# Performance work log

Hardware: AMD Instinct MI355X
Metric: run time of the kernel (lower is better)

The kernel has to match this reference:

```python
import jax, jax.numpy as jnp
import numpy as np

E = 128       # embed_dim
H = 128       # hidden_dim
NLABEL = 5
VOCAB = 50000
DEPTH = 18    # levels 0..17, complete binary tree
BRANCH = 2
N_NODES = 2 ** DEPTH - 1  # level-order layout: level l occupies [2^l-1, 2^(l+1)-1)


def setup_inputs() -> dict:
    key = jax.random.key(0)
    ks = jax.random.split(key, 24)

    def w(k, shape):
        return jax.random.normal(k, shape, dtype=jnp.float32) * 0.05

    inp = {
        "embeds": w(ks[0], (VOCAB, E)),
        "node_words": jax.random.randint(ks[1], (N_NODES,), 0, VOCAB),
        "node_labels": jax.random.randint(ks[2], (N_NODES,), 0, NLABEL),
        "depth": DEPTH,
        "branching": BRANCH,
    }
    # 8 gate linears: *x maps E->H, *h maps H->H (torch nn.Linear: y = x @ W.T + b)
    for j, nm in enumerate(["ix", "ih", "fx", "fh", "ox", "oh", "ux", "uh"]):
        in_dim = E if nm.endswith("x") else H
        inp["W" + nm] = w(ks[3 + 2 * j], (H, in_dim))
        inp["b" + nm] = w(ks[4 + 2 * j], (H,))
    inp["Wout"] = w(ks[20], (NLABEL, H))
    inp["bout"] = w(ks[21], (NLABEL,))
    return inp


def _lin(x, W, b):
    return x @ W.T + b


def _tree_lstm(embeds, node_words, node_labels, depth, branching,
               Wix, bix, Wih, bih, Wfx, bfx, Wfh, bfh,
               Wox, box, Woh, boh, Wux, bux, Wuh, buh, Wout, bout):
    b = branching
    hid = Wix.shape[0]
    loss = jnp.zeros((), dtype=embeds.dtype)
    child_c = child_h = None
    logp = None
    # bottom-up over levels (leaves first); level l has b^l nodes at offset (b^l-1)/(b-1)
    for l in range(depth - 1, -1, -1):
        n = b ** l
        off = (b ** l - 1) // (b - 1)
        x = embeds[node_words[off:off + n]]            # [n, E]
        if child_h is None:                            # leaves: zero child states
            h_sum = jnp.zeros((n, hid), dtype=embeds.dtype)
            c_agg = jnp.zeros((n, hid), dtype=embeds.dtype)
        else:
            ch = child_h.reshape(n, b, hid)            # children of each level-l node
            cc = child_c.reshape(n, b, hid)
            h_sum = ch.sum(axis=1)                     # child-sum
            f = jax.nn.sigmoid(_lin(x, Wfx, bfx)[:, None, :] + _lin(ch, Wfh, bfh))
            c_agg = (f * cc).sum(axis=1)               # sum_k f_k * c_k
        i = jax.nn.sigmoid(_lin(x, Wix, bix) + _lin(h_sum, Wih, bih))
        o = jax.nn.sigmoid(_lin(x, Wox, box) + _lin(h_sum, Woh, boh))
        u = jnp.tanh(_lin(x, Wux, bux) + _lin(h_sum, Wuh, buh))
        c = i * u + c_agg
        h = o * jnp.tanh(c)
        logp = jax.nn.log_softmax(_lin(h, Wout, bout), axis=-1)   # [n, NLABEL]
        lab = node_labels[off:off + n]
        loss = loss - logp[jnp.arange(n), lab].sum()              # NLL summed over nodes
        child_c, child_h = c, h
    return logp, loss  # logp from level 0 = root log-probs [1, NLABEL]


def reference(embeds, node_words, node_labels, depth, branching,
              Wix, bix, Wih, bih, Wfx, bfx, Wfh, bfh,
              Wox, box, Woh, boh, Wux, bux, Wuh, buh, Wout, bout):
    return _tree_lstm(embeds, node_words, node_labels, depth, branching,
                      Wix, bix, Wih, bih, Wfx, bfx, Wfh, bfh,
                      Wox, box, Woh, boh, Wux, bux, Wuh, buh, Wout, bout)
```

## Files before the change

### kernel.cpp

```cpp
#include <hip/hip_runtime.h>
#include <math.h>

#define DEPTH 18
#define NINT ((1 << (DEPTH - 1)) - 1)
#define LEAF_OFF ((1 << (DEPTH - 2)) - 1)
#define NVOCAB 50000
#define SAW 520
#define KTS 9

typedef unsigned short bf16raw;
typedef __bf16 bf16x8 __attribute__((ext_vector_type(8)));
typedef float f32x4 __attribute__((ext_vector_type(4)));
typedef short short8 __attribute__((ext_vector_type(8)));

__device__ __forceinline__ float sigm(float x) { return 1.0f / (1.0f + __expf(-x)); }
__device__ __forceinline__ float fast_tanh(float x) {
    float t = __expf(2.0f * x);
    return 1.0f - 2.0f / (t + 1.0f);
}

__device__ __forceinline__ float bf2f(bf16raw u) {
    union { unsigned int i; float f; } v;
    v.i = ((unsigned int)u) << 16;
    return v.f;
}
__device__ __forceinline__ bf16raw f2bf(float f) {
    union { float f; unsigned int i; } v;
    v.f = f;
    unsigned int r = v.i + 0x7FFFu + ((v.i >> 16) & 1u);
    return (bf16raw)(r >> 16);
}

#define SB() __builtin_amdgcn_sched_barrier(0)

__global__ __launch_bounds__(256) void k_prep_embeds(const float* __restrict__ src,
                                                     bf16raw* __restrict__ dst, int n4)
{
    int i = blockIdx.x * blockDim.x + threadIdx.x;
    if (i < n4) {
        float4 v = ((const float4*)src)[i];
        ushort4 o;
        o.x = f2bf(v.x); o.y = f2bf(v.y); o.z = f2bf(v.z); o.w = f2bf(v.w);
        ((ushort4*)dst)[i] = o;
    }
}

__global__ __launch_bounds__(128) void k_prep_bcat(
    const float* __restrict__ Wix, const float* __restrict__ bix,
    const float* __restrict__ Wih, const float* __restrict__ bih,
    const float* __restrict__ Wfx, const float* __restrict__ bfx,
    const float* __restrict__ Wfh, const float* __restrict__ bfh,
    const float* __restrict__ Wox, const float* __restrict__ box_,
    const float* __restrict__ Woh, const float* __restrict__ boh,
    const float* __restrict__ Wux, const float* __restrict__ bux,
    const float* __restrict__ Wuh, const float* __restrict__ buh,
    const float* __restrict__ Wout,
    bf16raw* __restrict__ Bfrag, bf16raw* __restrict__ WoutFrag,
    float* __restrict__ bias_cat)
{
    const int j = blockIdx.x;
    if (j >= 512) {
        const int col = j - 512;
        for (int k = threadIdx.x; k < 128; k += blockDim.x) {
            float v = (col < 5) ? Wout[col * 128 + k] : 0.f;
            WoutFrag[((k >> 5) * 64 + ((k >> 3) & 3) * 16 + col) * 8 + (k & 7)] = f2bf(v);
        }
        return;
    }
    const int gate = j >> 7, jj = j & 127;
    const float *Wx, *Wh, *bx, *bh;
    switch (gate) {
        case 0: Wx = Wix; Wh = Wih; bx = bix;  bh = bih; break;
        case 1: Wx = Wux; Wh = Wuh; bx = bux;  bh = buh; break;
        case 2: Wx = Wox; Wh = Woh; bx = box_; bh = boh; break;
        default: Wx = Wfx; Wh = Wfh; bx = bfx; bh = bfh; break;
    }
    const int coltile = (j >> 4) & 7, lr = j & 15;
    for (int k = threadIdx.x; k < 256; k += blockDim.x) {
        float v = (k < 128) ? Wx[jj * 128 + k] : Wh[jj * 128 + (k - 128)];
        const int idx = (((gate * 8 + coltile) * KTS + (k >> 5)) * 64
                         + ((k >> 3) & 3) * 16 + lr) * 8 + (k & 7);
        Bfrag[idx] = f2bf(v);
    }
    if (threadIdx.x == 0) bias_cat[j] = bx[jj] + bh[jj];
}

template<int CB>
__device__ __forceinline__ void lp_burst(const bf16raw* __restrict__ bfbase, int wcol,
                                         bf16x8 (&bb)[16])
{
#pragma unroll
    for (int kt = 0; kt < 4; ++kt)
#pragma unroll
        for (int j = 0; j < 4; ++j)
            bb[kt * 4 + j] = *(const bf16x8*)(bfbase +
                    (long)(((CB * 8 + (wcol >> 4) + j) * KTS + kt) * 512));
}

__device__ __forceinline__ void lp_mfma_all(const bf16raw* __restrict__ sA, int wrow,
                                            int lrow, int lquad,
                                            bf16x8 (&bb)[16], f32x4 (&acc)[2][4])
{
#pragma unroll
    for (int kt = 0; kt < 4; ++kt) {
        bf16x8 af[2];
#pragma unroll
        for (int i = 0; i < 2; ++i)
            af[i] = *(const bf16x8*)&sA[(wrow + i * 16 + lrow) * 136 + kt * 32 + lquad * 8];
#pragma unroll
        for (int i = 0; i < 2; ++i)
#pragma unroll
            for (int j = 0; j < 4; ++j)
                acc[i][j] = __builtin_amdgcn_mfma_f32_16x16x32_bf16(af[i], bb[kt * 4 + j], acc[i][j], 0, 0, 0);
    }
}

template<int CB>
__device__ __forceinline__ void lp_rungemm(const bf16raw* __restrict__ sA,
                                           const bf16raw* __restrict__ bfbase,
                                           int wrow, int wcol, int lrow, int lquad,
                                           f32x4 (&acc)[2][4])
{
#pragma unroll
    for (int i = 0; i < 2; i++)
#pragma unroll
        for (int j = 0; j < 4; j++) acc[i][j] = (f32x4){0.f, 0.f, 0.f, 0.f};
    bf16x8 bb[16];
    lp_burst<CB>(bfbase, wcol, bb);
    SB();
    lp_mfma_all(sA, wrow, lrow, lquad, bb, acc);
}

template<int G, int H>
__device__ __forceinline__ void load8(const bf16raw* __restrict__ bfbase, int w,
                                      bf16x8 (&bb)[8])
{
#pragma unroll
    for (int kt2 = 0; kt2 < 4; ++kt2)
#pragma unroll
        for (int jj = 0; jj < 2; ++jj)
            bb[kt2 * 2 + jj] = *(const bf16x8*)(bfbase +
                    (long)(((G * 8 + w * 2 + jj) * KTS + H * 4 + kt2) * 512));
}

template<int AB>
__device__ __forceinline__ void mfma4k(const bf16raw* __restrict__ sA, int lrow, int lquad,
                                       bf16x8 (&bb)[8], f32x4 (&acc)[2][2])
{
#pragma unroll
    for (int kt2 = 0; kt2 < 4; ++kt2) {
        bf16x8 af[2];
#pragma unroll
        for (int i = 0; i < 2; ++i)
            af[i] = *(const bf16x8*)&sA[(i * 16 + lrow) * SAW + (AB + kt2) * 32 + lquad * 8];
#pragma unroll
        for (int jj = 0; jj < 2; ++jj)
#pragma unroll
            for (int i = 0; i < 2; ++i)
                acc[i][jj] = __builtin_amdgcn_mfma_f32_16x16x32_bf16(af[i], bb[kt2 * 2 + jj], acc[i][jj], 0, 0, 0);
    }
}

__global__ __launch_bounds__(256, 3) void k_leafpre(
    const bf16raw* __restrict__ embeds_bf,
    const bf16raw* __restrict__ Bfrag, const float* __restrict__ bias_cat,
    const float* __restrict__ Wout, const float* __restrict__ bout,
    bf16raw* __restrict__ hc_leaf, float* __restrict__ lossv6, int nvtot)
{
    const int vbase = blockIdx.x * 64;
    int nv = nvtot - vbase;
    if (nv > 64) nv = 64;
    if (nv <= 0) return;

    __shared__ __align__(16) bf16raw sA[64 * 136];
    __shared__ __align__(16) bf16raw sT[64 * 136];
    __shared__ float sWout[5 * 128];

    const int t = threadIdx.x;
    for (int i = t; i < 640; i += 256) sWout[i] = Wout[i];

    {
        const int row = t >> 2;
        const int co = (t & 3) * 32;
        const int arow = (row < nv) ? row : 0;
        const bf16raw* ax = embeds_bf + (long)(vbase + arow) * 128;
        *(short8*)&sA[row * 136 + co]      = *(const short8*)(ax + co);
        *(short8*)&sA[row * 136 + co + 8]  = *(const short8*)(ax + co + 8);
        *(short8*)&sA[row * 136 + co + 16] = *(const short8*)(ax + co + 16);
        *(short8*)&sA[row * 136 + co + 24] = *(const short8*)(ax + co + 24);
    }

    const int lane = t & 63;
    const int w = t >> 6;
    const int wrow = (w & 1) * 32;
    const int wcol = (w >> 1) * 64;
    const int lrow = lane & 15;
    const int lquad = lane >> 4;

    __syncthreads();

    const bf16raw* bfbase = Bfrag + (long)lane * 8;

    float tval[2][4][4];
    f32x4 acc[2][4];

    lp_rungemm<0>(sA, bfbase, wrow, wcol, lrow, lquad, acc);
#pragma unroll
    for (int i = 0; i < 2; i++)
#pragma unroll
        for (int jj = 0; jj < 4; jj++) {
            const float b = bias_cat[wcol + jj * 16 + lrow];
#pragma unroll
            for (int r = 0; r < 4; r++) tval[i][jj][r] = sigm(acc[i][jj][r] + b);
        }
    lp_rungemm<1>(sA, bfbase, wrow, wcol, lrow, lquad, acc);
#pragma unroll
    for (int i = 0; i < 2; i++)
#pragma unroll
        for (int jj = 0; jj < 4; jj++) {
            const float b = bias_cat[128 + wcol + jj * 16 + lrow];
#pragma unroll
            for (int r = 0; r < 4; r++) tval[i][jj][r] *= fast_tanh(acc[i][jj][r] + b);
        }
#pragma unroll
    for (int i = 0; i < 2; i++)
#pragma unroll
        for (int jj = 0; jj < 4; jj++)
#pragma unroll
            for (int r = 0; r < 4; r++) {
                const int m = wrow + i * 16 + lquad * 4 + r;
                const int j = wcol + jj * 16 + lrow;
                sT[m * 136 + j] = f2bf(tval[i][jj][r]);
            }
#pragma unroll
    for (int i = 0; i < 2; i++)
#pragma unroll
        for (int jj = 0; jj < 4; jj++)
#pragma unroll
            for (int r = 0; r < 4; r++) tval[i][jj][r] = fast_tanh(tval[i][jj][r]);
    __syncthreads();
#pragma unroll
    for (int s = 0; s < 4; ++s) {
        int ci = t + 256 * s;
        int row = ci >> 4, c8 = (ci & 15) * 8;
        if (row < nv)
            *(short8*)(hc_leaf + (long)(vbase + row) * 256 + 128 + c8) = *(const short8*)&sT[row * 136 + c8];
    }
    lp_rungemm<2>(sA, bfbase, wrow, wcol, lrow, lquad, acc);
    __syncthreads();
#pragma unroll
    for (int i = 0; i < 2; i++)
#pragma unroll
        for (int jj = 0; jj < 4; jj++) {
            const float b = bias_cat[256 + wcol + jj * 16 + lrow];
#pragma unroll
            for (int r = 0; r < 4; r++) {
                const int m = wrow + i * 16 + lquad * 4 + r;
                const int j = wcol + jj * 16 + lrow;
                sT[m * 136 + j] = f2bf(sigm(acc[i][jj][r] + b) * tval[i][jj][r]);
            }
        }
    __syncthreads();
#pragma unroll
    for (int s = 0; s < 4; ++s) {
        int ci = t + 256 * s;
        int row = ci >> 4, c8 = (ci & 15) * 8;
        if (row < nv)
            *(short8*)(hc_leaf + (long)(vbase + row) * 256 + c8) = *(const short8*)&sT[row * 136 + c8];
    }
    {
        const int row = t >> 2, q = t & 3;
        float p[5] = {0.f, 0.f, 0.f, 0.f, 0.f};
        for (int k0 = 0; k0 < 32; ++k0) {
            const int k = q * 32 + k0;
            float hv = bf2f(sT[row * 136 + k]);
#pragma unroll
            for (int l = 0; l < 5; l++) p[l] += hv * sWout[l * 128 + k];
        }
#pragma unroll
        for (int l = 0; l < 5; l++) {
            p[l] += __shfl_down(p[l], 2);
            p[l] += __shfl_down(p[l], 1);
        }
        if (q == 0 && row < nv) {
            float lg[5], mx = -1e30f;
#pragma unroll
            for (int l = 0; l < 5; l++) {
                lg[l] = p[l] + bout[l];
                mx = fmaxf(mx, lg[l]);
            }
            float se = 0.f;
#pragma unroll
            for (int l = 0; l < 5; l++) se += __expf(lg[l] - mx);
            float lse = __logf(se) + mx;
            float* dst = lossv6 + (long)(vbase + row) * 6;
#pragma unroll
            for (int l = 0; l < 5; l++) dst[l] = lg[l];
            dst[5] = lse;
        }
    }
}

__global__ __launch_bounds__(256, 3) void k_level32(
    const bf16raw* __restrict__ embeds_bf, const int* __restrict__ words,
    const int* __restrict__ labels,
    bf16raw* __restrict__ h_all, bf16raw* __restrict__ c_all,
    const bf16raw* __restrict__ hc_leaf, const float* __restrict__ lossv6,
    const bf16raw* __restrict__ Bfrag, const bf16raw* __restrict__ WoutFrag,
    const float* __restrict__ bias_cat, const float* __restrict__ bout,
    float* __restrict__ partials, float* __restrict__ out,
    int off, int nm, int leafkids, int isroot)
{
    __shared__ __align__(16) bf16raw sA[32 * SAW];
    __shared__ __align__(16) bf16raw sCT[64 * 136];
    __shared__ float sLg[32 * 5];

    const int t = threadIdx.x;
    const int m0 = blockIdx.x * 32;

    {
        const int row = t >> 3;
        const int co = (t & 7) * 8;
        int mm = m0 + row; if (mm >= nm) mm = nm - 1;
        const long g = (long)off + mm;
        const bf16raw* px = embeds_bf + (long)words[g] * 128;
        const bf16raw *p1, *p2;
        if (leafkids) {
            p1 = hc_leaf + (long)words[2 * g + 1] * 256;
            p2 = hc_leaf + (long)words[2 * g + 2] * 256;
        } else {
            p1 = h_all + (2 * g + 1) * 128;
            p2 = h_all + (2 * g + 2) * 128;
        }
        short8 vx0 = *(const short8*)(px + co);
        short8 vx1 = *(const short8*)(px + 64 + co);
        short8 h10 = *(const short8*)(p1 + co);
        short8 h11 = *(const short8*)(p1 + 64 + co);
        short8 h20 = *(const short8*)(p2 + co);
        short8 h21 = *(const short8*)(p2 + 64 + co);
        short8 hs0, hs1;
#pragma unroll
        for (int e = 0; e < 8; ++e) {
            hs0[e] = (short)f2bf(bf2f((bf16raw)(unsigned short)h10[e]) +
                                 bf2f((bf16raw)(unsigned short)h20[e]));
            hs1[e] = (short)f2bf(bf2f((bf16raw)(unsigned short)h11[e]) +
                                 bf2f((bf16raw)(unsigned short)h21[e]));
        }
        *(short8*)&sA[row * SAW + co]        = vx0;
        *(short8*)&sA[row * SAW + 64 + co]   = vx1;
        *(short8*)&sA[row * SAW + 128 + co]  = hs0;
        *(short8*)&sA[row * SAW + 192 + co]  = hs1;
        *(short8*)&sA[row * SAW + 256 + co]  = h10;
        *(short8*)&sA[row * SAW + 320 + co]  = h11;
        *(short8*)&sA[row * SAW + 384 + co]  = h20;
        *(short8*)&sA[row * SAW + 448 + co]  = h21;
    }
    {
        const int slot = t >> 2;
        const int cc8 = (t & 3) * 8;
        int mm = m0 + (slot >> 1); if (mm >= nm) mm = nm - 1;
        const long g = (long)off + mm;
        const long cg = 2 * g + 1 + (slot & 1);
        const bf16raw* pc = leafkids ? (hc_leaf + (long)words[cg] * 256 + 128)
                                     : (c_all + cg * 128);
#pragma unroll
        for (int s = 0; s < 4; ++s)
            *(short8*)&sCT[slot * 136 + s * 32 + cc8] = *(const short8*)(pc + s * 32 + cc8);
    }

    const int lane = t & 63;
    const int w = t >> 6;
    const int lrow = lane & 15;
    const int lquad = lane >> 4;

    float bias[4][2];
#pragma unroll
    for (int g = 0; g < 4; ++g)
#pragma unroll
        for (int jj = 0; jj < 2; ++jj)
            bias[g][jj] = bias_cat[g * 128 + w * 32 + jj * 16 + lrow];

    __syncthreads();

    const bf16raw* bfbase = Bfrag + (long)lane * 8;

    f32x4 acc[2][2];
    f32x4 fx[2][2];
    float si[2][2][4];
    float cc[2][2][4];
    float hh[2][2][4];
    bf16x8 bbA[8], bbB[8];

#define ZACC() { _Pragma("unroll") for (int i_ = 0; i_ < 2; ++i_) \
                 _Pragma("unroll") for (int j_ = 0; j_ < 2; ++j_) \
                     acc[i_][j_] = (f32x4){0.f, 0.f, 0.f, 0.f}; }

    load8<0, 0>(bfbase, w, bbA);
    load8<0, 1>(bfbase, w, bbB);
    SB();
    ZACC();
    mfma4k<0>(sA, lrow, lquad, bbA, acc); SB();
    load8<1, 0>(bfbase, w, bbA); SB();
    mfma4k<4>(sA, lrow, lquad, bbB, acc); SB();
    load8<1, 1>(bfbase, w, bbB); SB();
#pragma unroll
    for (int i = 0; i < 2; ++i)
#pragma unroll
        for (int jj = 0; jj < 2; ++jj)
#pragma unroll
            for (int r = 0; r < 4; ++r)
                si[i][jj][r] = sigm(acc[i][jj][r] + bias[0][jj]);
    ZACC();
    mfma4k<0>(sA, lrow, lquad, bbA, acc); SB();
    load8<3, 0>(bfbase, w, bbA); SB();
    mfma4k<4>(sA, lrow, lquad, bbB, acc); SB();
    load8<3, 1>(bfbase, w, bbB); SB();
#pragma unroll
    for (int i = 0; i < 2; ++i)
#pragma unroll
        for (int jj = 0; jj < 2; ++jj)
#pragma unroll
            for (int r = 0; r < 4; ++r)
                cc[i][jj][r] = si[i][jj][r] * fast_tanh(acc[i][jj][r] + bias[1][jj]);
    ZACC();
    mfma4k<0>(sA, lrow, lquad, bbA, acc);
    SB();
#pragma unroll
    for (int i = 0; i < 2; ++i)
#pragma unroll
        for (int jj = 0; jj < 2; ++jj) fx[i][jj] = acc[i][jj];
    mfma4k<8>(sA, lrow, lquad, bbB, acc);
    SB();
    load8<2, 0>(bfbase, w, bbA);
    SB();
#pragma unroll
    for (int i = 0; i < 2; ++i)
#pragma unroll
        for (int jj = 0; jj < 2; ++jj) {
            const int j = w * 32 + jj * 16 + lrow;
#pragma unroll
            for (int r = 0; r < 4; ++r) {
                const int m = i * 16 + lquad * 4 + r;
                cc[i][jj][r] += sigm(acc[i][jj][r] + bias[3][jj]) * bf2f(sCT[(2 * m) * 136 + j]);
            }
        }
#pragma unroll
    for (int i = 0; i < 2; ++i)
#pragma unroll
        for (int jj = 0; jj < 2; ++jj) acc[i][jj] = fx[i][jj];
    mfma4k<12>(sA, lrow, lquad, bbB, acc);
    SB();
    load8<2, 1>(bfbase, w, bbB);
    SB();
#pragma unroll
    for (int i = 0; i < 2; ++i)
#pragma unroll
        for (int jj = 0; jj < 2; ++jj) {
            const int j = w * 32 + jj * 16 + lrow;
#pragma unroll
            for (int r = 0; r < 4; ++r) {
                const int m = i * 16 + lquad * 4 + r;
                cc[i][jj][r] += sigm(acc[i][jj][r] + bias[3][jj]) * bf2f(sCT[(2 * m + 1) * 136 + j]);
            }
        }
    ZACC();
    mfma4k<0>(sA, lrow, lquad, bbA, acc);
    mfma4k<4>(sA, lrow, lquad, bbB, acc);
    SB();
#pragma unroll
    for (int i = 0; i < 2; ++i)
#pragma unroll
        for (int jj = 0; jj < 2; ++jj)
#pragma unroll
            for (int r = 0; r < 4; ++r)
                hh[i][jj][r] = sigm(acc[i][jj][r] + bias[2][jj]) * fast_tanh(cc[i][jj][r]);
#undef ZACC

    __syncthreads();

#pragma unroll
    for (int i = 0; i < 2; ++i)
#pragma unroll
        for (int jj = 0; jj < 2; ++jj) {
            const int j = w * 32 + jj * 16 + lrow;
#pragma unroll
            for (int r = 0; r < 4; ++r) {
                const int m = i * 16 + lquad * 4 + r;
                sCT[m * 136 + j] = f2bf(cc[i][jj][r]);
                sCT[(32 + m) * 136 + j] = f2bf(hh[i][jj][r]);
            }
        }
    __syncthreads();

#pragma unroll
    for (int q = 0; q < 4; ++q) {
        int ci = t + 256 * q;
        int row = ci >> 4;
        int c8 = (ci & 15) * 8;
        int m = row & 31;
        if (m0 + m < nm) {
            bf16raw* dst = (row < 32) ? c_all : h_all;
            *(short8*)(dst + ((long)off + m0 + m) * 128 + c8) = *(const short8*)&sCT[row * 136 + c8];
        }
    }

    if (w == 0) {
        f32x4 lacc[2];
        lacc[0] = (f32x4){0.f, 0.f, 0.f, 0.f};
        lacc[1] = (f32x4){0.f, 0.f, 0.f, 0.f};
#pragma unroll
        for (int kt = 0; kt < 4; ++kt) {
            bf16x8 bfr = *(const bf16x8*)(WoutFrag + (long)((kt * 64 + lane) * 8));
#pragma unroll
            for (int i = 0; i < 2; ++i) {
                bf16x8 af = *(const bf16x8*)&sCT[(32 + i * 16 + lrow) * 136 + kt * 32 + lquad * 8];
                lacc[i] = __builtin_amdgcn_mfma_f32_16x16x32_bf16(af, bfr, lacc[i], 0, 0, 0);
            }
        }
        if (lrow < 5) {
            const float bl = bout[lrow];
#pragma unroll
            for (int i = 0; i < 2; ++i)
#pragma unroll
                for (int r = 0; r < 4; ++r)
                    sLg[(i * 16 + lquad * 4 + r) * 5 + lrow] = lacc[i][r] + bl;
        }
    }
    __syncthreads();

    if (t < 32 && m0 + t < nm) {
        const long g = (long)off + m0 + t;
        float lgv[5], mx = -1e30f;
#pragma unroll
        for (int l = 0; l < 5; ++l) {
            lgv[l] = sLg[t * 5 + l];
            mx = fmaxf(mx, lgv[l]);
        }
        float se = 0.f;
#pragma unroll
        for (int l = 0; l < 5; ++l) se += __expf(lgv[l] - mx);
        float lse = __logf(se) + mx;
        float lossNode = lse - lgv[labels[g]];
        if (leafkids) {
            const float* lv1 = lossv6 + (long)words[2 * g + 1] * 6;
            const float* lv2 = lossv6 + (long)words[2 * g + 2] * 6;
            lossNode += (lv1[5] - lv1[labels[2 * g + 1]])
                      + (lv2[5] - lv2[labels[2 * g + 2]]);
        }
        atomicAdd(&partials[(int)(g & 1023)], lossNode);
        if (isroot && g == 0) {
#pragma unroll
            for (int l = 0; l < 5; ++l) out[l] = lgv[l] - lse;
        }
    }
}

__global__ __launch_bounds__(256) void k3_reduce(const float* __restrict__ partials,
                                                 float* __restrict__ out)
{
    const int t = threadIdx.x;
    float s = 0.f;
    for (int i = t; i < 1024; i += 256) s += partials[i];
#pragma unroll
    for (int d = 32; d > 0; d >>= 1) s += __shfl_down(s, d);
    __shared__ float red[4];
    if ((t & 63) == 0) red[t >> 6] = s;
    __syncthreads();
    if (t == 0) out[5] = red[0] + red[1] + red[2] + red[3];
}

extern "C" void kernel_launch(void* const* d_in, const int* in_sizes, int n_in,
                              void* d_out, int out_size, void* d_ws, size_t ws_size,
                              hipStream_t stream)
{
    const float* embeds = (const float*)d_in[0];
    const int* words = (const int*)d_in[1];
    const int* labels = (const int*)d_in[2];
    const float* Wix = (const float*)d_in[5],  *bix  = (const float*)d_in[6];
    const float* Wih = (const float*)d_in[7],  *bih  = (const float*)d_in[8];
    const float* Wfx = (const float*)d_in[9],  *bfx  = (const float*)d_in[10];
    const float* Wfh = (const float*)d_in[11], *bfh  = (const float*)d_in[12];
    const float* Wox = (const float*)d_in[13], *box_ = (const float*)d_in[14];
    const float* Woh = (const float*)d_in[15], *boh  = (const float*)d_in[16];
    const float* Wux = (const float*)d_in[17], *bux  = (const float*)d_in[18];
    const float* Wuh = (const float*)d_in[19], *buh  = (const float*)d_in[20];
    const float* Wout = (const float*)d_in[21], *bout = (const float*)d_in[22];
    float* out = (float*)d_out;

    char* ws = (char*)d_ws;
    const size_t treeElems = (size_t)NINT * 128;
    bf16raw* h_all = (bf16raw*)ws;
    bf16raw* c_all = h_all + treeElems;
    bf16raw* embeds_bf = c_all + treeElems;
    bf16raw* Bfrag = embeds_bf + (size_t)NVOCAB * 128;
    bf16raw* WoutFrag = Bfrag + 4 * 8 * KTS * 512;
    bf16raw* hc_leaf = WoutFrag + 4 * 64 * 8;
    float* lossv6 = (float*)(hc_leaf + (size_t)NVOCAB * 256);
    float* bias_cat = lossv6 + (size_t)NVOCAB * 6;
    float* partials = bias_cat + 512;

    k_prep_embeds<<<(NVOCAB * 128 / 4 + 255) / 256, 256, 0, stream>>>(
        embeds, embeds_bf, NVOCAB * 128 / 4);
    k_prep_bcat<<<528, 128, 0, stream>>>(Wix, bix, Wih, bih, Wfx, bfx, Wfh, bfh,
                                         Wox, box_, Woh, boh, Wux, bux, Wuh, buh,
                                         Wout, Bfrag, WoutFrag, bias_cat);
    hipMemsetAsync(partials, 0, 1024 * sizeof(float), stream);

    k_leafpre<<<(NVOCAB + 63) / 64, 256, 0, stream>>>(
        embeds_bf, Bfrag, bias_cat, Wout, bout, hc_leaf, lossv6, NVOCAB);

    for (int l = DEPTH - 2; l >= 0; --l) {
        const int n = 1 << l;
        k_level32<<<dim3((n + 31) / 32), 256, 0, stream>>>(
            embeds_bf, words, labels, h_all, c_all, hc_leaf, lossv6,
            Bfrag, WoutFrag, bias_cat, bout, partials, out,
            n - 1, n, (l == DEPTH - 2) ? 1 : 0, (l == 0) ? 1 : 0);
    }

    k3_reduce<<<1, 256, 0, stream>>>(partials, out);
}
```

Measured before the change: 371.4 us.

## Merge prep kernels, fold final reduce into root level, MFMA leaf logits

Merges the embedding conversion, weight-fragment packing and partials zeroing into one launch, and drops the separate memset. The final loss reduction now runs inside the root-level launch, removing the k3_reduce kernel. The leaf output projection uses an MFMA over the prebuilt WoutFrag instead of a scalar dot loop. The goal is less per-launch overhead on a chain of small kernels. The root-level reduce depends on earlier atomics being visible across kernel boundaries, which holds because the launches are stream-ordered.

Measured after the change: 366.5 us. About the same (-1.3%).

```diff
diff --git a/kernel.cpp b/kernel.cpp
--- a/kernel.cpp
+++ b/kernel.cpp
@@ -7,6 +7,7 @@
 #define NVOCAB 50000
 #define SAW 520
 #define KTS 9
+#define NEMB (NVOCAB * 128 / 4 / 256)
 
 typedef unsigned short bf16raw;
 typedef __bf16 bf16x8 __attribute__((ext_vector_type(8)));
@@ -33,19 +34,8 @@
 
 #define SB() __builtin_amdgcn_sched_barrier(0)
 
-__global__ __launch_bounds__(256) void k_prep_embeds(const float* __restrict__ src,
-                                                     bf16raw* __restrict__ dst, int n4)
-{
-    int i = blockIdx.x * blockDim.x + threadIdx.x;
-    if (i < n4) {
-        float4 v = ((const float4*)src)[i];
-        ushort4 o;
-        o.x = f2bf(v.x); o.y = f2bf(v.y); o.z = f2bf(v.z); o.w = f2bf(v.w);
-        ((ushort4*)dst)[i] = o;
-    }
-}
-
-__global__ __launch_bounds__(128) void k_prep_bcat(
+__global__ __launch_bounds__(256) void k_prep_all(
+    const float* __restrict__ embeds,
     const float* __restrict__ Wix, const float* __restrict__ bix,
     const float* __restrict__ Wih, const float* __restrict__ bih,
     const float* __restrict__ Wfx, const float* __restrict__ bfx,
@@ -55,13 +45,29 @@
     const float* __restrict__ Wux, const float* __restrict__ bux,
     const float* __restrict__ Wuh, const float* __restrict__ buh,
     const float* __restrict__ Wout,
+    bf16raw* __restrict__ embeds_bf,
     bf16raw* __restrict__ Bfrag, bf16raw* __restrict__ WoutFrag,
-    float* __restrict__ bias_cat)
-{
-    const int j = blockIdx.x;
+    float* __restrict__ bias_cat, float* __restrict__ partials)
+{
+    const int bid = blockIdx.x;
+    const int t = threadIdx.x;
+    if (bid < NEMB) {
+        const int i = bid * 256 + t;
+        float4 v = ((const float4*)embeds)[i];
+        ushort4 o;
+        o.x = f2bf(v.x); o.y = f2bf(v.y); o.z = f2bf(v.z); o.w = f2bf(v.w);
+        ((ushort4*)embeds_bf)[i] = o;
+        return;
+    }
+    if (bid == NEMB + 528) {
+#pragma unroll
+        for (int s = 0; s < 4; ++s) partials[t + 256 * s] = 0.f;
+        return;
+    }
+    const int j = bid - NEMB;
     if (j >= 512) {
         const int col = j - 512;
-        for (int k = threadIdx.x; k < 128; k += blockDim.x) {
+        for (int k = t; k < 128; k += 256) {
             float v = (col < 5) ? Wout[col * 128 + k] : 0.f;
             WoutFrag[((k >> 5) * 64 + ((k >> 3) & 3) * 16 + col) * 8 + (k & 7)] = f2bf(v);
         }
@@ -76,13 +82,13 @@
         default: Wx = Wfx; Wh = Wfh; bx = bfx; bh = bfh; break;
     }
     const int coltile = (j >> 4) & 7, lr = j & 15;
-    for (int k = threadIdx.x; k < 256; k += blockDim.x) {
+    for (int k = t; k < 256; k += 256) {
         float v = (k < 128) ? Wx[jj * 128 + k] : Wh[jj * 128 + (k - 128)];
         const int idx = (((gate * 8 + coltile) * KTS + (k >> 5)) * 64
                          + ((k >> 3) & 3) * 16 + lr) * 8 + (k & 7);
         Bfrag[idx] = f2bf(v);
     }
-    if (threadIdx.x == 0) bias_cat[j] = bx[jj] + bh[jj];
+    if (t == 0) bias_cat[j] = bx[jj] + bh[jj];
 }
 
 template<int CB>
@@ -164,7 +170,7 @@
 __global__ __launch_bounds__(256, 3) void k_leafpre(
     const bf16raw* __restrict__ embeds_bf,
     const bf16raw* __restrict__ Bfrag, const float* __restrict__ bias_cat,
-    const float* __restrict__ Wout, const float* __restrict__ bout,
+    const bf16raw* __restrict__ WoutFrag, const float* __restrict__ bout,
     bf16raw* __restrict__ hc_leaf, float* __restrict__ lossv6, int nvtot)
 {
     const int vbase = blockIdx.x * 64;
@@ -174,10 +180,9 @@
 
     __shared__ __align__(16) bf16raw sA[64 * 136];
     __shared__ __align__(16) bf16raw sT[64 * 136];
-    __shared__ float sWout[5 * 128];
+    __shared__ float sLg[64 * 5];
 
     const int t = threadIdx.x;
-    for (int i = t; i < 640; i += 256) sWout[i] = Wout[i];
 
     {
         const int row = t >> 2;
@@ -269,35 +274,36 @@
             *(short8*)(hc_leaf + (long)(vbase + row) * 256 + c8) = *(const short8*)&sT[row * 136 + c8];
     }
     {
-        const int row = t >> 2, q = t & 3;
-        float p[5] = {0.f, 0.f, 0.f, 0.f, 0.f};
-        for (int k0 = 0; k0 < 32; ++k0) {
-            const int k = q * 32 + k0;
-            float hv = bf2f(sT[row * 136 + k]);
-#pragma unroll
-            for (int l = 0; l < 5; l++) p[l] += hv * sWout[l * 128 + k];
-        }
+        f32x4 lacc = (f32x4){0.f, 0.f, 0.f, 0.f};
+#pragma unroll
+        for (int kt = 0; kt < 4; ++kt) {
+            bf16x8 bfr = *(const bf16x8*)(WoutFrag + (long)((kt * 64 + lane) * 8));
+            bf16x8 af = *(const bf16x8*)&sT[(w * 16 + lrow) * 136 + kt * 32 + lquad * 8];
+            lacc = __builtin_amdgcn_mfma_f32_16x16x32_bf16(af, bfr, lacc, 0, 0, 0);
+        }
+        if (lrow < 5) {
+            const float bl = bout[lrow];
+#pragma unroll
+            for (int r = 0; r < 4; ++r)
+                sLg[(w * 16 + lquad * 4 + r) * 5 + lrow] = lacc[r] + bl;
+        }
+    }
+    __syncthreads();
+    if (t < 64 && t < nv) {
+        float lg[5], mx = -1e30f;
 #pragma unroll
         for (int l = 0; l < 5; l++) {
-            p[l] += __shfl_down(p[l], 2);
-            p[l] += __shfl_down(p[l], 1);
-        }
-        if (q == 0 && row < nv) {
-            float lg[5], mx = -1e30f;
-#pragma unroll
-            for (int l = 0; l < 5; l++) {
-                lg[l] = p[l] + bout[l];
-                mx = fmaxf(mx, lg[l]);
-            }
-            float se = 0.f;
-#pragma unroll
-            for (int l = 0; l < 5; l++) se += __expf(lg[l] - mx);
-            float lse = __logf(se) + mx;
-            float* dst = lossv6 + (long)(vbase + row) * 6;
-#pragma unroll
-            for (int l = 0; l < 5; l++) dst[l] = lg[l];
-            dst[5] = lse;
-        }
+            lg[l] = sLg[t * 5 + l];
+            mx = fmaxf(mx, lg[l]);
+        }
+        float se = 0.f;
+#pragma unroll
+        for (int l = 0; l < 5; l++) se += __expf(lg[l] - mx);
+        float lse = __logf(se) + mx;
+        float* dst = lossv6 + (long)(vbase + t) * 6;
+#pragma unroll
+        for (int l = 0; l < 5; l++) dst[l] = lg[l];
+        dst[5] = lse;
     }
 }
 
@@ -313,7 +319,7 @@
 {
     __shared__ __align__(16) bf16raw sA[32 * SAW];
     __shared__ __align__(16) bf16raw sCT[64 * 136];
-    __shared__ float sLg[32 * 5];
+    __shared__ float sLg[168];
 
     const int t = threadIdx.x;
     const int m0 = blockIdx.x * 32;
@@ -547,26 +553,26 @@
             lossNode += (lv1[5] - lv1[labels[2 * g + 1]])
                       + (lv2[5] - lv2[labels[2 * g + 2]]);
         }
-        atomicAdd(&partials[(int)(g & 1023)], lossNode);
-        if (isroot && g == 0) {
+        if (isroot) {
+            sLg[164] = lossNode;
 #pragma unroll
             for (int l = 0; l < 5; ++l) out[l] = lgv[l] - lse;
-        }
-    }
-}
-
-__global__ __launch_bounds__(256) void k3_reduce(const float* __restrict__ partials,
-                                                 float* __restrict__ out)
-{
-    const int t = threadIdx.x;
-    float s = 0.f;
-    for (int i = t; i < 1024; i += 256) s += partials[i];
-#pragma unroll
-    for (int d = 32; d > 0; d >>= 1) s += __shfl_down(s, d);
-    __shared__ float red[4];
-    if ((t & 63) == 0) red[t >> 6] = s;
-    __syncthreads();
-    if (t == 0) out[5] = red[0] + red[1] + red[2] + red[3];
+        } else {
+            atomicAdd(&partials[(int)(g & 1023)], lossNode);
+        }
+    }
+
+    if (isroot) {
+        __syncthreads();
+        float s = 0.f;
+        for (int i2 = t; i2 < 1024; i2 += 256) s += partials[i2];
+#pragma unroll
+        for (int d = 32; d > 0; d >>= 1) s += __shfl_down(s, d);
+        if ((t & 63) == 0) sLg[160 + (t >> 6)] = s;
+        __syncthreads();
+        if (t == 0)
+            out[5] = sLg[160] + sLg[161] + sLg[162] + sLg[163] + sLg[164];
+    }
 }
 
 extern "C" void kernel_launch(void* const* d_in, const int* in_sizes, int n_in,
@@ -599,15 +605,13 @@
     float* bias_cat = lossv6 + (size_t)NVOCAB * 6;
     float* partials = bias_cat + 512;
 
-    k_prep_embeds<<<(NVOCAB * 128 / 4 + 255) / 256, 256, 0, stream>>>(
-        embeds, embeds_bf, NVOCAB * 128 / 4);
-    k_prep_bcat<<<528, 128, 0, stream>>>(Wix, bix, Wih, bih, Wfx, bfx, Wfh, bfh,
-                                         Wox, box_, Woh, boh, Wux, bux, Wuh, buh,
-                                         Wout, Bfrag, WoutFrag, bias_cat);
-    hipMemsetAsync(partials, 0, 1024 * sizeof(float), stream);
+    k_prep_all<<<NEMB + 528 + 1, 256, 0, stream>>>(
+        embeds, Wix, bix, Wih, bih, Wfx, bfx, Wfh, bfh,
+        Wox, box_, Woh, boh, Wux, bux, Wuh, buh, Wout,
+        embeds_bf, Bfrag, WoutFrag, bias_cat, partials);
 
     k_leafpre<<<(NVOCAB + 63) / 64, 256, 0, stream>>>(
-        embeds_bf, Bfrag, bias_cat, Wout, bout, hc_leaf, lossv6, NVOCAB);
+        embeds_bf, Bfrag, bias_cat, WoutFrag, bout, hc_leaf, lossv6, NVOCAB);
 
     for (int l = DEPTH - 2; l >= 0; --l) {
         const int n = 1 << l;
@@ -616,6 +620,4 @@
             Bfrag, WoutFrag, bias_cat, bout, partials, out,
             n - 1, n, (l == DEPTH - 2) ? 1 : 0, (l == 0) ? 1 : 0);
     }
-
-    k3_reduce<<<1, 256, 0, stream>>>(partials, out);
-}
+}
```
